# Kernel tuning notes

Measured on AMD Instinct MI355X. Metric: run time of the kernel, lower is better.

The kernel has to match this reference:

```python
import jax, jax.numpy as jnp
import numpy as np

B, L, HID = 2, 2048, 2048
H, KVH, HD = 8, 1, 256
GROUPS = H // KVH
THETA = 10000.0
NEG_INF = -1e9


def _rope_cos_sin(seq_len, hd):
    inv_freq = 1.0 / (THETA ** (jnp.arange(0, hd, 2, dtype=jnp.float32) / hd))
    t = jnp.arange(seq_len, dtype=jnp.float32)
    freqs = jnp.outer(t, inv_freq)                # [L, hd/2]
    emb = jnp.concatenate([freqs, freqs], axis=-1)  # [L, hd]
    return jnp.cos(emb), jnp.sin(emb)


def _rotate_half(x):
    x1, x2 = jnp.split(x, 2, axis=-1)
    return jnp.concatenate([-x2, x1], axis=-1)


def _apply_rope(x, cos, sin):
    # x: [B, h, L, hd]; cos/sin: [L, hd] broadcast over batch/heads
    return x * cos[None, None] + _rotate_half(x) * sin[None, None]


def setup_inputs() -> dict:
    key = jax.random.key(0)
    kx, kq, kk, kv, ko = jax.random.split(key, 5)
    s = lambda fan_in: 1.0 / np.sqrt(fan_in)
    x = jax.random.normal(kx, (B, L, HID), dtype=jnp.float32)
    Wq = jax.random.normal(kq, (HID, H * HD), dtype=jnp.float32) * s(HID)
    Wk = jax.random.normal(kk, (HID, KVH * HD), dtype=jnp.float32) * s(HID)
    Wv = jax.random.normal(kv, (HID, KVH * HD), dtype=jnp.float32) * s(HID)
    Wo = jax.random.normal(ko, (H * HD, HID), dtype=jnp.float32) * s(H * HD)
    # causal additive mask, same semantics as SDPA attn_mask (float, additive)
    causal = jnp.tril(jnp.ones((L, L), dtype=bool))
    mask = jnp.where(causal, 0.0, NEG_INF).astype(jnp.float32)[None, None]
    return {"x": x, "Wq": Wq, "Wk": Wk, "Wv": Wv, "Wo": Wo, "mask": mask}


def reference(x, Wq, Wk, Wv, Wo, mask):
    # projections -> [B, h, L, hd]
    q = (x @ Wq).reshape(B, L, H, HD).transpose(0, 2, 1, 3)
    k = (x @ Wk).reshape(B, L, KVH, HD).transpose(0, 2, 1, 3)
    v = (x @ Wv).reshape(B, L, KVH, HD).transpose(0, 2, 1, 3)
    cos, sin = _rope_cos_sin(L, HD)
    q = _apply_rope(q, cos, sin)
    k = _apply_rope(k, cos, sin)
    # GQA: replicate kv heads (repeat_interleave over head dim)
    k = jnp.repeat(k, GROUPS, axis=1)
    v = jnp.repeat(v, GROUPS, axis=1)
    scale = HD ** -0.5
    scores = jnp.einsum("bhqd,bhkd->bhqk", q, k) * scale + mask
    attn = jax.nn.softmax(scores.astype(jnp.float32), axis=-1).astype(q.dtype)
    out = jnp.einsum("bhqk,bhkd->bhqd", attn, v)
    out = out.transpose(0, 2, 1, 3).reshape(B, L, H * HD)
    return out @ Wo
```

## Files before the change

### kernel.cpp

```cpp
#include <hip/hip_runtime.h>

typedef unsigned short u16;
typedef __attribute__((ext_vector_type(8))) short short8x;
typedef __attribute__((ext_vector_type(4))) float f32x4;

#define B_ 2
#define L_ 2048
#define HID_ 2048
#define H_ 8
#define HD_ 256

__device__ __forceinline__ u16 f2bf(float f) {
  union { float f; unsigned u; } v; v.f = f;
  unsigned r = v.u + 0x7FFFu + ((v.u >> 16) & 1u);
  return (u16)(r >> 16);
}
__device__ __forceinline__ float bf2f(u16 u) {
  union { unsigned u; float f; } v; v.u = ((unsigned)u) << 16;
  return v.f;
}

__device__ __forceinline__ void gload_lds16(const void* g, void* l) {
  __builtin_amdgcn_global_load_lds((const __attribute__((address_space(1))) unsigned*)g,
                                   (__attribute__((address_space(3))) unsigned*)l, 16, 0, 0);
}

__global__ __launch_bounds__(256) void cvt_x_kernel(const float4* __restrict__ in,
                                                    u16* __restrict__ out) {
  int idx = blockIdx.x * 256 + threadIdx.x;
  float4 v = in[idx];
  u16* o = out + (size_t)idx * 4;
  o[0] = f2bf(v.x); o[1] = f2bf(v.y); o[2] = f2bf(v.z); o[3] = f2bf(v.w);
}

__global__ __launch_bounds__(256) void cvt_wt_kernel(const float* __restrict__ W,
                                                     u16* __restrict__ Wt, int K, int N) {
  __shared__ float tile[32][33];
  int n0 = blockIdx.x * 32, k0 = blockIdx.y * 32;
  int tx = threadIdx.x, ty = threadIdx.y;
#pragma unroll
  for (int i = 0; i < 32; i += 8)
    tile[ty + i][tx] = W[(size_t)(k0 + ty + i) * N + n0 + tx];
  __syncthreads();
#pragma unroll
  for (int i = 0; i < 32; i += 8)
    Wt[(size_t)(n0 + ty + i) * K + k0 + tx] = f2bf(tile[tx][ty + i]);
}

__global__ __launch_bounds__(256) void rope_kernel(const u16* __restrict__ in,
                                                   u16* __restrict__ out, int nh_shift,
                                                   int in_stride, int in_off, float scale) {
  int idx = blockIdx.x * 256 + threadIdx.x;
  int nh = 1 << nh_shift;
  int d = idx & 127;
  int t = idx >> 7;
  int h = t & (nh - 1);
  int row = t >> nh_shift;
  int l = row & (L_ - 1);
  int b = row >> 11;
  size_t ibase = (size_t)row * in_stride + in_off + h * 256 + d;
  float x1 = bf2f(in[ibase]);
  float x2 = bf2f(in[ibase + 128]);
  float f = exp2f(-(float)d * (13.287712379549449f / 128.0f));
  float ang = (float)l * f;
  float s, c;
  sincosf(ang, &s, &c);
  size_t obase = ((size_t)(b * nh + h) * L_ + l) * 256 + d;
  out[obase] = f2bf((x1 * c - x2 * s) * scale);
  out[obase + 128] = f2bf((x2 * c + x1 * s) * scale);
}

__global__ __launch_bounds__(256) void vt_kernel(const u16* __restrict__ qkvproj,
                                                 u16* __restrict__ vt) {
  __shared__ u16 tile[32][33];
  int l0 = blockIdx.x * 32, d0 = blockIdx.y * 32, b = blockIdx.z;
  int tx = threadIdx.x, ty = threadIdx.y;
#pragma unroll
  for (int i = 0; i < 32; i += 8)
    tile[ty + i][tx] = qkvproj[((size_t)b * 2048 + l0 + ty + i) * 2560 + 2304 + d0 + tx];
  __syncthreads();
#pragma unroll
  for (int i = 0; i < 32; i += 8)
    vt[((size_t)b * 256 + d0 + ty + i) * 2048 + l0 + tx] = tile[tx][ty + i];
}

template <int F32OUT>
__global__ __launch_bounds__(512) void gemm256_kernel(const u16* __restrict__ A,
                                                      const u16* __restrict__ Bt,
                                                      void* __restrict__ Cv,
                                                      int M, int N, int K) {
  __shared__ __attribute__((aligned(16))) u16 As[2][256 * 64];
  __shared__ __attribute__((aligned(16))) u16 Bs[2][256 * 64];
  const int tid = threadIdx.x, lane = tid & 63, w = tid >> 6;
  const int wr = w >> 2, wc = w & 3;
  const int l15 = lane & 15, l4 = lane >> 4;
  const int nbx = gridDim.x;
  int flat = blockIdx.y * nbx + blockIdx.x;
  int nwg = nbx * gridDim.y;
  int q8 = nwg >> 3, r8 = nwg & 7;
  int xcd = flat & 7, idx8 = flat >> 3;
  int neu = (xcd < r8 ? xcd * (q8 + 1) : r8 * (q8 + 1) + (xcd - r8) * q8) + idx8;
  const int m0 = (neu / nbx) * 256, n0 = (neu % nbx) * 256;
  const int NT = K >> 6;

  f32x4 acc[8][4] = {};
  short8x a[4][2], b[4][2];

#define STAGE_A(t, s)                                                           \
  {                                                                             \
    _Pragma("unroll") for (int i = 0; i < 4; ++i) {                             \
      int c = i * 512 + tid;                                                    \
      int row = c >> 3, j = (c & 7) ^ (row & 7);                                \
      gload_lds16(A + (size_t)(m0 + row) * K + (t) * 64 + j * 8,                \
                  (char*)&As[s][0] + (i * 512 + w * 64) * 16);                  \
    }                                                                           \
  }
#define STAGE_B(t, s)                                                           \
  {                                                                             \
    _Pragma("unroll") for (int i = 0; i < 4; ++i) {                             \
      int c = i * 512 + tid;                                                    \
      int row = c >> 3, j = (c & 7) ^ (row & 7);                                \
      gload_lds16(Bt + (size_t)(n0 + row) * K + (t) * 64 + j * 8,               \
                  (char*)&Bs[s][0] + (i * 512 + w * 64) * 16);                  \
    }                                                                           \
  }
#define RD_A(s, mi, ks)                                                         \
  (*(const short8x*)((const char*)&As[s][0] +                                   \
      ((((wr * 128 + (mi) * 16 + l15) * 128 + ((ks) * 4 + l4) * 16)) ^          \
       ((l15 & 7) << 4))))
#define RD_B(s, ni, ks)                                                         \
  (*(const short8x*)((const char*)&Bs[s][0] +                                   \
      ((((wc * 64 + (ni) * 16 + l15) * 128 + ((ks) * 4 + l4) * 16)) ^           \
       ((l15 & 7) << 4))))

  STAGE_A(0, 0);
  STAGE_B(0, 0);
  asm volatile("s_waitcnt vmcnt(0)" ::: "memory");
  __builtin_amdgcn_s_barrier();

  for (int t = 0; t < NT; ++t) {
    const int s = t & 1;
    const bool ns = (t + 1 < NT);
#pragma unroll
    for (int mi = 0; mi < 4; ++mi) { a[mi][0] = RD_A(s, mi, 0); a[mi][1] = RD_A(s, mi, 1); }
#pragma unroll
    for (int ni = 0; ni < 2; ++ni) { b[ni][0] = RD_B(s, ni, 0); b[ni][1] = RD_B(s, ni, 1); }
    if (ns) STAGE_A(t + 1, s ^ 1);
    __builtin_amdgcn_s_barrier();
    __builtin_amdgcn_s_setprio(1);
#pragma unroll
    for (int mi = 0; mi < 4; ++mi)
#pragma unroll
      for (int ni = 0; ni < 2; ++ni) {
        acc[mi][ni] = __builtin_amdgcn_mfma_f32_16x16x32_bf16(a[mi][0], b[ni][0], acc[mi][ni], 0, 0, 0);
        acc[mi][ni] = __builtin_amdgcn_mfma_f32_16x16x32_bf16(a[mi][1], b[ni][1], acc[mi][ni], 0, 0, 0);
      }
    __builtin_amdgcn_s_setprio(0);
    __builtin_amdgcn_s_barrier();
#pragma unroll
    for (int ni = 2; ni < 4; ++ni) { b[ni][0] = RD_B(s, ni, 0); b[ni][1] = RD_B(s, ni, 1); }
    if (ns) STAGE_B(t + 1, s ^ 1);
    __builtin_amdgcn_s_barrier();
    __builtin_amdgcn_s_setprio(1);
#pragma unroll
    for (int mi = 0; mi < 4; ++mi)
#pragma unroll
      for (int ni = 2; ni < 4; ++ni) {
        acc[mi][ni] = __builtin_amdgcn_mfma_f32_16x16x32_bf16(a[mi][0], b[ni][0], acc[mi][ni], 0, 0, 0);
        acc[mi][ni] = __builtin_amdgcn_mfma_f32_16x16x32_bf16(a[mi][1], b[ni][1], acc[mi][ni], 0, 0, 0);
      }
    __builtin_amdgcn_s_setprio(0);
    __builtin_amdgcn_s_barrier();
#pragma unroll
    for (int mi = 0; mi < 4; ++mi) { a[mi][0] = RD_A(s, mi + 4, 0); a[mi][1] = RD_A(s, mi + 4, 1); }
    __builtin_amdgcn_s_barrier();
    __builtin_amdgcn_s_setprio(1);
#pragma unroll
    for (int mi = 0; mi < 4; ++mi)
#pragma unroll
      for (int ni = 2; ni < 4; ++ni) {
        acc[mi + 4][ni] = __builtin_amdgcn_mfma_f32_16x16x32_bf16(a[mi][0], b[ni][0], acc[mi + 4][ni], 0, 0, 0);
        acc[mi + 4][ni] = __builtin_amdgcn_mfma_f32_16x16x32_bf16(a[mi][1], b[ni][1], acc[mi + 4][ni], 0, 0, 0);
      }
    __builtin_amdgcn_s_setprio(0);
    __builtin_amdgcn_s_barrier();
    __builtin_amdgcn_s_setprio(1);
#pragma unroll
    for (int mi = 0; mi < 4; ++mi)
#pragma unroll
      for (int ni = 0; ni < 2; ++ni) {
        acc[mi + 4][ni] = __builtin_amdgcn_mfma_f32_16x16x32_bf16(a[mi][0], b[ni][0], acc[mi + 4][ni], 0, 0, 0);
        acc[mi + 4][ni] = __builtin_amdgcn_mfma_f32_16x16x32_bf16(a[mi][1], b[ni][1], acc[mi + 4][ni], 0, 0, 0);
      }
    __builtin_amdgcn_s_setprio(0);
    if (ns) asm volatile("s_waitcnt vmcnt(0)" ::: "memory");
    __builtin_amdgcn_s_barrier();
  }
#pragma unroll
  for (int mi = 0; mi < 8; ++mi) {
#pragma unroll
    for (int ni = 0; ni < 4; ++ni) {
      int gcol = n0 + wc * 64 + ni * 16 + l15;
#pragma unroll
      for (int r = 0; r < 4; ++r) {
        int grow = m0 + wr * 128 + mi * 16 + l4 * 4 + r;
        if (F32OUT)
          ((float*)Cv)[(size_t)grow * N + gcol] = acc[mi][ni][r];
        else
          ((u16*)Cv)[(size_t)grow * N + gcol] = f2bf(acc[mi][ni][r]);
      }
    }
  }
#undef STAGE_A
#undef STAGE_B
#undef RD_A
#undef RD_B
}

__global__ __launch_bounds__(512) void flash_kernel(const u16* __restrict__ qb,
                                                    const u16* __restrict__ kb,
                                                    const u16* __restrict__ vt,
                                                    u16* __restrict__ attn_o) {
  __shared__ __attribute__((aligned(16))) u16 Kbuf[2][64 * 256];
  __shared__ __attribute__((aligned(16))) u16 Vbuf[2][256 * 64];
  __shared__ __attribute__((aligned(16))) u16 Ps[8 * 16 * 64];
  const int x = blockIdx.x;
  const int p = x >> 4;
  const int bh = x & 15;
  const int b = bh >> 3;
  const int h = bh & 7;
  const int tid = threadIdx.x, lane = tid & 63, w = tid >> 6;
  const int l15 = lane & 15, l4 = lane >> 4;
  const int j = (w < 4) ? (31 - p) : p;
  const int q0 = j * 64 + (w & 3) * 16;
  const int nt = (31 - p) + 1;

  const u16* qrow = qb + ((size_t)(b * 8 + h) * L_ + q0 + l15) * 256;
  short8x qf[8];
#pragma unroll
  for (int kc = 0; kc < 8; ++kc)
    qf[kc] = *(const short8x*)(qrow + kc * 32 + l4 * 8);

  f32x4 o[16] = {};
  float mrow = -3e38f, srow = 0.f;

  const u16* kbase = kb + (size_t)b * (L_ * 256);
  const u16* vbase = vt + (size_t)b * (256 * L_);

#define STAGE(t, s)                                                            \
  {                                                                            \
    _Pragma("unroll") for (int i2 = 0; i2 < 4; ++i2) {                         \
      int c = i2 * 512 + tid;                                                  \
      int rk = c >> 5, cck = c & 31, jk = cck ^ (rk & 7);                      \
      gload_lds16(kbase + (size_t)((t) * 64 + rk) * 256 + jk * 8,              \
                  (char*)&Kbuf[s][0] + (i2 * 512 + w * 64) * 16);              \
      int rd = c >> 3, ccv = c & 7, jv = ccv ^ (rd & 7);                       \
      gload_lds16(vbase + (size_t)rd * L_ + (t) * 64 + jv * 8,                 \
                  (char*)&Vbuf[s][0] + (i2 * 512 + w * 64) * 16);              \
    }                                                                          \
  }

  STAGE(0, 0);
  asm volatile("s_waitcnt vmcnt(0)" ::: "memory");
  __syncthreads();

  for (int t = 0; t < nt; ++t) {
    if (t + 1 < nt) STAGE(t + 1, (t + 1) & 1);
    if (t <= j) {
      const char* Kb = (const char*)&Kbuf[t & 1][0];
      const char* Vb = (const char*)&Vbuf[t & 1][0];

      f32x4 sacc[4] = {};
      __builtin_amdgcn_s_setprio(1);
#pragma unroll
      for (int kc = 0; kc < 8; ++kc)
#pragma unroll
        for (int n = 0; n < 4; ++n) {
          int row = n * 16 + l15;
          short8x kf = *(const short8x*)(Kb +
              ((row * 512 + kc * 64 + l4 * 16) ^ ((row & 7) << 4)));
          sacc[n] = __builtin_amdgcn_mfma_f32_16x16x32_bf16(kf, qf[kc], sacc[n], 0, 0, 0);
        }
      __builtin_amdgcn_s_setprio(0);
      float pp[4][4];
      const bool dm = (t == j);
      const int qg = q0 + l15;
      float pm = -3e38f;
#pragma unroll
      for (int n = 0; n < 4; ++n)
#pragma unroll
        for (int r = 0; r < 4; ++r) {
          int kvg = t * 64 + n * 16 + l4 * 4 + r;
          float v = sacc[n][r];
          if (dm && (kvg > qg)) v = -1e30f;
          pp[n][r] = v;
          pm = fmaxf(pm, v);
        }
      pm = fmaxf(pm, __shfl_xor(pm, 16));
      pm = fmaxf(pm, __shfl_xor(pm, 32));
      const bool defer = __all(pm <= mrow + 8.f);
      float mn, alpha;
      if (defer) {
        mn = mrow;
      } else {
        mn = fmaxf(mrow, pm);
        alpha = __expf(mrow - mn);
        mrow = mn;
      }
      float rs = 0.f;
#pragma unroll
      for (int n = 0; n < 4; ++n)
#pragma unroll
        for (int r = 0; r < 4; ++r) {
          pp[n][r] = __expf(pp[n][r] - mn);
          rs += pp[n][r];
        }
      rs += __shfl_xor(rs, 16);
      rs += __shfl_xor(rs, 32);
      if (defer) {
        srow += rs;
      } else {
        srow = srow * alpha + rs;
        float av[4];
#pragma unroll
        for (int r = 0; r < 4; ++r)
          av[r] = __shfl(alpha, l4 * 4 + r, 16);
#pragma unroll
        for (int ff = 0; ff < 16; ++ff) {
          o[ff][0] *= av[0]; o[ff][1] *= av[1];
          o[ff][2] *= av[2]; o[ff][3] *= av[3];
        }
      }
#pragma unroll
      for (int n = 0; n < 4; ++n)
#pragma unroll
        for (int r = 0; r < 4; r += 2) {
          unsigned pk;
          asm("v_cvt_pk_bf16_f32 %0, %1, %2" : "=v"(pk) : "v"(pp[n][r]), "v"(pp[n][r + 1]));
          *(unsigned*)((char*)Ps + w * 2048 +
                       ((l15 * 128 + (n * 16 + l4 * 4 + r) * 2) ^ ((l15 & 7) << 4))) = pk;
        }
      asm volatile("s_waitcnt lgkmcnt(0)" ::: "memory");
      short8x paf[2];
#pragma unroll
      for (int kc2 = 0; kc2 < 2; ++kc2)
        paf[kc2] = *(const short8x*)((const char*)Ps + w * 2048 +
            ((l15 * 128 + kc2 * 64 + l4 * 16) ^ ((l15 & 7) << 4)));
      __builtin_amdgcn_s_setprio(1);
#pragma unroll
      for (int kc2 = 0; kc2 < 2; ++kc2)
#pragma unroll
        for (int ff = 0; ff < 16; ++ff) {
          int rd = ff * 16 + l15;
          short8x vf = *(const short8x*)(Vb +
              ((rd * 128 + kc2 * 64 + l4 * 16) ^ ((rd & 7) << 4)));
          o[ff] = __builtin_amdgcn_mfma_f32_16x16x32_bf16(paf[kc2], vf, o[ff], 0, 0, 0);
        }
      __builtin_amdgcn_s_setprio(0);
    }
    asm volatile("s_waitcnt vmcnt(0)" ::: "memory");
    __syncthreads();
  }
  float sv[4];
#pragma unroll
  for (int r = 0; r < 4; ++r)
    sv[r] = __shfl(srow, l4 * 4 + r, 16);
#pragma unroll
  for (int r = 0; r < 4; ++r) {
    float inv = 1.0f / sv[r];
    int grow = q0 + l4 * 4 + r;
    size_t base = ((size_t)b * L_ + grow) * (size_t)(H_ * HD_) + h * 256;
#pragma unroll
    for (int ff = 0; ff < 16; ++ff)
      attn_o[base + ff * 16 + l15] = f2bf(o[ff][r] * inv);
  }
#undef STAGE
}

extern "C" void kernel_launch(void* const* d_in, const int* in_sizes, int n_in,
                              void* d_out, int out_size, void* d_ws, size_t ws_size,
                              hipStream_t stream) {
  const float* x  = (const float*)d_in[0];
  const float* Wq = (const float*)d_in[1];
  const float* Wk = (const float*)d_in[2];
  const float* Wv = (const float*)d_in[3];
  const float* Wo = (const float*)d_in[4];
  float* out = (float*)d_out;
  char* ws = (char*)d_ws;
  size_t off = 0;
  auto alloc = [&](size_t bytes) {
    void* p = ws + off;
    off = (off + bytes + 255) & ~(size_t)255;
    return p;
  };
  u16* wqkv_t  = (u16*)alloc(2560ull * 2048 * 2);
  u16* wo_t    = (u16*)alloc(2048ull * 2048 * 2);
  u16* xbf     = (u16*)alloc(4096ull * 2048 * 2);
  u16* qkvproj = (u16*)alloc(4096ull * 2560 * 2);
  u16* kb      = (u16*)alloc(4096ull * 256 * 2);
  u16* vtb     = (u16*)alloc(4096ull * 256 * 2);
  u16* qbuf    = xbf;
  u16* attn_o  = qkvproj;

  cvt_x_kernel<<<8192, 256, 0, stream>>>((const float4*)x, xbf);
  cvt_wt_kernel<<<dim3(64, 64), dim3(32, 8), 0, stream>>>(Wq, wqkv_t, 2048, 2048);
  cvt_wt_kernel<<<dim3(8, 64),  dim3(32, 8), 0, stream>>>(Wk, wqkv_t + 2048ull * 2048, 2048, 256);
  cvt_wt_kernel<<<dim3(8, 64),  dim3(32, 8), 0, stream>>>(Wv, wqkv_t + 2304ull * 2048, 2048, 256);
  cvt_wt_kernel<<<dim3(64, 64), dim3(32, 8), 0, stream>>>(Wo, wo_t, 2048, 2048);

  gemm256_kernel<0><<<dim3(10, 16), 512, 0, stream>>>(xbf, wqkv_t, qkvproj, 4096, 2560, 2048);

  rope_kernel<<<16384, 256, 0, stream>>>(qkvproj, qbuf, 3, 2560, 0, 0.0625f);
  rope_kernel<<<2048, 256, 0, stream>>>(qkvproj, kb, 0, 2560, 2048, 1.0f);
  vt_kernel<<<dim3(64, 8, 2), dim3(32, 8), 0, stream>>>(qkvproj, vtb);

  flash_kernel<<<256, 512, 0, stream>>>(qbuf, kb, vtb, attn_o);

  gemm256_kernel<1><<<dim3(8, 16), 512, 0, stream>>>(attn_o, wo_t, out, 4096, 2048, 2048);
}
```

Measured before the change: 242.0 us.

## Switch GEMMs to 256x128 tiles with triple-buffered LDS prefetch

Replaces the 256x256-tile GEMM with a 256x128 tile. The 8 waves now form a 4x2 grid, each computing a 64x64 sub-tile. Shared buffers go from double to triple buffering, so loads for tile t+2 are issued while tile t is computed, with a partial vmcnt wait. The grid doubles, giving 320 and 256 workgroups on 256 CUs instead of 160 and 128, which is meant to fill the GPU better and hide global latency. The trade-off is lower arithmetic intensity per tile, more LDS per block (144KB), and vmcnt counts that must match the number of issued loads.

```diff
diff --git a/kernel.cpp b/kernel.cpp
--- a/kernel.cpp
+++ b/kernel.cpp
@@ -85,14 +85,14 @@
 }
 
 template <int F32OUT>
-__global__ __launch_bounds__(512) void gemm256_kernel(const u16* __restrict__ A,
-                                                      const u16* __restrict__ Bt,
-                                                      void* __restrict__ Cv,
-                                                      int M, int N, int K) {
-  __shared__ __attribute__((aligned(16))) u16 As[2][256 * 64];
-  __shared__ __attribute__((aligned(16))) u16 Bs[2][256 * 64];
+__global__ __launch_bounds__(512) void gemmtb_kernel(const u16* __restrict__ A,
+                                                     const u16* __restrict__ Bt,
+                                                     void* __restrict__ Cv,
+                                                     int M, int N, int K) {
+  __shared__ __attribute__((aligned(16))) u16 As[3][256 * 64];
+  __shared__ __attribute__((aligned(16))) u16 Bs[3][128 * 64];
   const int tid = threadIdx.x, lane = tid & 63, w = tid >> 6;
-  const int wr = w >> 2, wc = w & 3;
+  const int wr = w >> 1, wc = w & 1;
   const int l15 = lane & 15, l4 = lane >> 4;
   const int nbx = gridDim.x;
   int flat = blockIdx.y * nbx + blockIdx.x;
@@ -100,10 +100,10 @@
   int q8 = nwg >> 3, r8 = nwg & 7;
   int xcd = flat & 7, idx8 = flat >> 3;
   int neu = (xcd < r8 ? xcd * (q8 + 1) : r8 * (q8 + 1) + (xcd - r8) * q8) + idx8;
-  const int m0 = (neu / nbx) * 256, n0 = (neu % nbx) * 256;
+  const int m0 = (neu / nbx) * 256, n0 = (neu % nbx) * 128;
   const int NT = K >> 6;
 
-  f32x4 acc[8][4] = {};
+  f32x4 acc[4][4] = {};
   short8x a[4][2], b[4][2];
 
 #define STAGE_A(t, s)                                                           \
@@ -117,7 +117,7 @@
   }
 #define STAGE_B(t, s)                                                           \
   {                                                                             \
-    _Pragma("unroll") for (int i = 0; i < 4; ++i) {                             \
+    _Pragma("unroll") for (int i = 0; i < 2; ++i) {                             \
       int c = i * 512 + tid;                                                    \
       int row = c >> 3, j = (c & 7) ^ (row & 7);                                \
       gload_lds16(Bt + (size_t)(n0 + row) * K + (t) * 64 + j * 8,               \
@@ -126,7 +126,7 @@
   }
 #define RD_A(s, mi, ks)                                                         \
   (*(const short8x*)((const char*)&As[s][0] +                                   \
-      ((((wr * 128 + (mi) * 16 + l15) * 128 + ((ks) * 4 + l4) * 16)) ^          \
+      ((((wr * 64 + (mi) * 16 + l15) * 128 + ((ks) * 4 + l4) * 16)) ^           \
        ((l15 & 7) << 4))))
 #define RD_B(s, ni, ks)                                                         \
   (*(const short8x*)((const char*)&Bs[s][0] +                                   \
@@ -135,17 +135,19 @@
 
   STAGE_A(0, 0);
   STAGE_B(0, 0);
-  asm volatile("s_waitcnt vmcnt(0)" ::: "memory");
+  STAGE_A(1, 1);
+  STAGE_B(1, 1);
+  asm volatile("s_waitcnt vmcnt(6)" ::: "memory");
   __builtin_amdgcn_s_barrier();
 
   for (int t = 0; t < NT; ++t) {
-    const int s = t & 1;
-    const bool ns = (t + 1 < NT);
-#pragma unroll
-    for (int mi = 0; mi < 4; ++mi) { a[mi][0] = RD_A(s, mi, 0); a[mi][1] = RD_A(s, mi, 1); }
-#pragma unroll
-    for (int ni = 0; ni < 2; ++ni) { b[ni][0] = RD_B(s, ni, 0); b[ni][1] = RD_B(s, ni, 1); }
-    if (ns) STAGE_A(t + 1, s ^ 1);
+    const int cur = t % 3, nxt = (t + 2) % 3;
+    const bool ns = (t + 2 < NT);
+#pragma unroll
+    for (int mi = 0; mi < 4; ++mi) { a[mi][0] = RD_A(cur, mi, 0); a[mi][1] = RD_A(cur, mi, 1); }
+#pragma unroll
+    for (int ni = 0; ni < 2; ++ni) { b[ni][0] = RD_B(cur, ni, 0); b[ni][1] = RD_B(cur, ni, 1); }
+    if (ns) STAGE_A(t + 2, nxt);
     __builtin_amdgcn_s_barrier();
     __builtin_amdgcn_s_setprio(1);
 #pragma unroll
@@ -158,8 +160,8 @@
     __builtin_amdgcn_s_setprio(0);
     __builtin_amdgcn_s_barrier();
 #pragma unroll
-    for (int ni = 2; ni < 4; ++ni) { b[ni][0] = RD_B(s, ni, 0); b[ni][1] = RD_B(s, ni, 1); }
-    if (ns) STAGE_B(t + 1, s ^ 1);
+    for (int ni = 2; ni < 4; ++ni) { b[ni][0] = RD_B(cur, ni, 0); b[ni][1] = RD_B(cur, ni, 1); }
+    if (ns) STAGE_B(t + 2, nxt);
     __builtin_amdgcn_s_barrier();
     __builtin_amdgcn_s_setprio(1);
 #pragma unroll
@@ -170,40 +172,18 @@
         acc[mi][ni] = __builtin_amdgcn_mfma_f32_16x16x32_bf16(a[mi][1], b[ni][1], acc[mi][ni], 0, 0, 0);
       }
     __builtin_amdgcn_s_setprio(0);
+    if (ns) asm volatile("s_waitcnt vmcnt(6)" ::: "memory");
+    else    asm volatile("s_waitcnt vmcnt(0)" ::: "memory");
     __builtin_amdgcn_s_barrier();
-#pragma unroll
-    for (int mi = 0; mi < 4; ++mi) { a[mi][0] = RD_A(s, mi + 4, 0); a[mi][1] = RD_A(s, mi + 4, 1); }
-    __builtin_amdgcn_s_barrier();
-    __builtin_amdgcn_s_setprio(1);
-#pragma unroll
-    for (int mi = 0; mi < 4; ++mi)
-#pragma unroll
-      for (int ni = 2; ni < 4; ++ni) {
-        acc[mi + 4][ni] = __builtin_amdgcn_mfma_f32_16x16x32_bf16(a[mi][0], b[ni][0], acc[mi + 4][ni], 0, 0, 0);
-        acc[mi + 4][ni] = __builtin_amdgcn_mfma_f32_16x16x32_bf16(a[mi][1], b[ni][1], acc[mi + 4][ni], 0, 0, 0);
-      }
-    __builtin_amdgcn_s_setprio(0);
-    __builtin_amdgcn_s_barrier();
-    __builtin_amdgcn_s_setprio(1);
-#pragma unroll
-    for (int mi = 0; mi < 4; ++mi)
-#pragma unroll
-      for (int ni = 0; ni < 2; ++ni) {
-        acc[mi + 4][ni] = __builtin_amdgcn_mfma_f32_16x16x32_bf16(a[mi][0], b[ni][0], acc[mi + 4][ni], 0, 0, 0);
-        acc[mi + 4][ni] = __builtin_amdgcn_mfma_f32_16x16x32_bf16(a[mi][1], b[ni][1], acc[mi + 4][ni], 0, 0, 0);
-      }
-    __builtin_amdgcn_s_setprio(0);
-    if (ns) asm volatile("s_waitcnt vmcnt(0)" ::: "memory");
-    __builtin_amdgcn_s_barrier();
-  }
-#pragma unroll
-  for (int mi = 0; mi < 8; ++mi) {
+  }
+#pragma unroll
+  for (int mi = 0; mi < 4; ++mi) {
 #pragma unroll
     for (int ni = 0; ni < 4; ++ni) {
       int gcol = n0 + wc * 64 + ni * 16 + l15;
 #pragma unroll
       for (int r = 0; r < 4; ++r) {
-        int grow = m0 + wr * 128 + mi * 16 + l4 * 4 + r;
+        int grow = m0 + wr * 64 + mi * 16 + l4 * 4 + r;
         if (F32OUT)
           ((float*)Cv)[(size_t)grow * N + gcol] = acc[mi][ni][r];
         else
@@ -408,7 +388,7 @@
   cvt_wt_kernel<<<dim3(8, 64),  dim3(32, 8), 0, stream>>>(Wv, wqkv_t + 2304ull * 2048, 2048, 256);
   cvt_wt_kernel<<<dim3(64, 64), dim3(32, 8), 0, stream>>>(Wo, wo_t, 2048, 2048);
 
-  gemm256_kernel<0><<<dim3(10, 16), 512, 0, stream>>>(xbf, wqkv_t, qkvproj, 4096, 2560, 2048);
+  gemmtb_kernel<0><<<dim3(20, 16), 512, 0, stream>>>(xbf, wqkv_t, qkvproj, 4096, 2560, 2048);
 
   rope_kernel<<<16384, 256, 0, stream>>>(qkvproj, qbuf, 3, 2560, 0, 0.0625f);
   rope_kernel<<<2048, 256, 0, stream>>>(qkvproj, kb, 0, 2560, 2048, 1.0f);
@@ -416,5 +396,5 @@
 
   flash_kernel<<<256, 512, 0, stream>>>(qbuf, kb, vtb, attn_o);
 
-  gemm256_kernel<1><<<dim3(8, 16), 512, 0, stream>>>(attn_o, wo_t, out, 4096, 2048, 2048);
-}
+  gemmtb_kernel<1><<<dim3(16, 16), 512, 0, stream>>>(attn_o, wo_t, out, 4096, 2048, 2048);
+}
```

Result: faster. 229.7 us (-5.1%).

## Split GEMM tiles into half-tiles and prefetch B two k-steps ahead

Applied to the files above, without the earlier changes.

Restructures the 256x256 GEMM kernel so the A and B LDS tiles are stored as two 128-row halves. Each half is staged at a separate point in the MFMA schedule, with B prefetched two k-steps ahead and partial vmcnt waits instead of full drains. The aim is to spread global-to-LDS traffic across the compute phases and hide load latency better, in the style of 8-phase ping-pong GEMM schedules. The cost is more complex synchronisation, where an error in the wait counts could cause reads of stale LDS data.

```diff
diff --git a/kernel.cpp b/kernel.cpp
--- a/kernel.cpp
+++ b/kernel.cpp
@@ -85,12 +85,12 @@
 }
 
 template <int F32OUT>
-__global__ __launch_bounds__(512) void gemm256_kernel(const u16* __restrict__ A,
-                                                      const u16* __restrict__ Bt,
-                                                      void* __restrict__ Cv,
-                                                      int M, int N, int K) {
-  __shared__ __attribute__((aligned(16))) u16 As[2][256 * 64];
-  __shared__ __attribute__((aligned(16))) u16 Bs[2][256 * 64];
+__global__ __launch_bounds__(512) void gemm8p_kernel(const u16* __restrict__ A,
+                                                     const u16* __restrict__ Bt,
+                                                     void* __restrict__ Cv,
+                                                     int M, int N, int K) {
+  __shared__ __attribute__((aligned(16))) u16 As[2][2][128 * 64];
+  __shared__ __attribute__((aligned(16))) u16 Bs[2][2][128 * 64];
   const int tid = threadIdx.x, lane = tid & 63, w = tid >> 6;
   const int wr = w >> 2, wc = w & 3;
   const int l15 = lane & 15, l4 = lane >> 4;
@@ -104,96 +104,102 @@
   const int NT = K >> 6;
 
   f32x4 acc[8][4] = {};
-  short8x a[4][2], b[4][2];
-
-#define STAGE_A(t, s)                                                           \
-  {                                                                             \
-    _Pragma("unroll") for (int i = 0; i < 4; ++i) {                             \
-      int c = i * 512 + tid;                                                    \
-      int row = c >> 3, j = (c & 7) ^ (row & 7);                                \
-      gload_lds16(A + (size_t)(m0 + row) * K + (t) * 64 + j * 8,                \
-                  (char*)&As[s][0] + (i * 512 + w * 64) * 16);                  \
-    }                                                                           \
-  }
-#define STAGE_B(t, s)                                                           \
-  {                                                                             \
-    _Pragma("unroll") for (int i = 0; i < 4; ++i) {                             \
-      int c = i * 512 + tid;                                                    \
-      int row = c >> 3, j = (c & 7) ^ (row & 7);                                \
-      gload_lds16(Bt + (size_t)(n0 + row) * K + (t) * 64 + j * 8,               \
-                  (char*)&Bs[s][0] + (i * 512 + w * 64) * 16);                  \
-    }                                                                           \
-  }
-#define RD_A(s, mi, ks)                                                         \
-  (*(const short8x*)((const char*)&As[s][0] +                                   \
-      ((((wr * 128 + (mi) * 16 + l15) * 128 + ((ks) * 4 + l4) * 16)) ^          \
-       ((l15 & 7) << 4))))
-#define RD_B(s, ni, ks)                                                         \
-  (*(const short8x*)((const char*)&Bs[s][0] +                                   \
-      ((((wc * 64 + (ni) * 16 + l15) * 128 + ((ks) * 4 + l4) * 16)) ^           \
-       ((l15 & 7) << 4))))
-
-  STAGE_A(0, 0);
-  STAGE_B(0, 0);
-  asm volatile("s_waitcnt vmcnt(0)" ::: "memory");
+  short8x a[4][2], blo[2][2], bhi[2][2];
+
+#define STAGE_HT(PTR, br, h, t, s, SBUF)                                          \
+  {                                                                               \
+    _Pragma("unroll") for (int i = 0; i < 2; ++i) {                               \
+      int c = i * 512 + tid;                                                      \
+      int row = c >> 3, j = (c & 7) ^ (row & 7);                                  \
+      gload_lds16(PTR + (size_t)((br) + (h) * 128 + row) * K + (t) * 64 + j * 8,  \
+                  (char*)&SBUF[s][h][0] + (i * 512 + w * 64) * 16);               \
+    }                                                                             \
+  }
+#define RD(SBUF, s, h, rowin, ks)                                                 \
+  (*(const short8x*)((const char*)&SBUF[s][h][0] +                                \
+      ((((rowin) * 128 + ((ks) * 4 + l4) * 16)) ^ (((rowin) & 7) << 4))))
+
+  const int brB = (wc & 1) * 64;
+
+  STAGE_HT(A, m0, 0, 0, 0, As);
+  STAGE_HT(A, m0, 1, 0, 0, As);
+  STAGE_HT(Bt, n0, 0, 0, 0, Bs);
+  STAGE_HT(Bt, n0, 1, 0, 0, Bs);
+  STAGE_HT(Bt, n0, 0, 1, 1, Bs);
+  STAGE_HT(Bt, n0, 1, 1, 1, Bs);
+  asm volatile("s_waitcnt vmcnt(4)" ::: "memory");
   __builtin_amdgcn_s_barrier();
 
   for (int t = 0; t < NT; ++t) {
-    const int s = t & 1;
-    const bool ns = (t + 1 < NT);
-#pragma unroll
-    for (int mi = 0; mi < 4; ++mi) { a[mi][0] = RD_A(s, mi, 0); a[mi][1] = RD_A(s, mi, 1); }
-#pragma unroll
-    for (int ni = 0; ni < 2; ++ni) { b[ni][0] = RD_B(s, ni, 0); b[ni][1] = RD_B(s, ni, 1); }
-    if (ns) STAGE_A(t + 1, s ^ 1);
+    const int s = t & 1, sn = s ^ 1;
+#pragma unroll
+    for (int mi = 0; mi < 4; ++mi) {
+      a[mi][0] = RD(As, s, wr, mi * 16 + l15, 0);
+      a[mi][1] = RD(As, s, wr, mi * 16 + l15, 1);
+    }
+#pragma unroll
+    for (int ni = 0; ni < 2; ++ni) {
+      blo[ni][0] = RD(Bs, s, wc >> 1, brB + ni * 16 + l15, 0);
+      blo[ni][1] = RD(Bs, s, wc >> 1, brB + ni * 16 + l15, 1);
+    }
+    if (t + 1 < NT) STAGE_HT(A, m0, 0, t + 1, sn, As);
     __builtin_amdgcn_s_barrier();
     __builtin_amdgcn_s_setprio(1);
 #pragma unroll
     for (int mi = 0; mi < 4; ++mi)
 #pragma unroll
       for (int ni = 0; ni < 2; ++ni) {
-        acc[mi][ni] = __builtin_amdgcn_mfma_f32_16x16x32_bf16(a[mi][0], b[ni][0], acc[mi][ni], 0, 0, 0);
-        acc[mi][ni] = __builtin_amdgcn_mfma_f32_16x16x32_bf16(a[mi][1], b[ni][1], acc[mi][ni], 0, 0, 0);
+        acc[mi][ni] = __builtin_amdgcn_mfma_f32_16x16x32_bf16(a[mi][0], blo[ni][0], acc[mi][ni], 0, 0, 0);
+        acc[mi][ni] = __builtin_amdgcn_mfma_f32_16x16x32_bf16(a[mi][1], blo[ni][1], acc[mi][ni], 0, 0, 0);
       }
     __builtin_amdgcn_s_setprio(0);
     __builtin_amdgcn_s_barrier();
 #pragma unroll
-    for (int ni = 2; ni < 4; ++ni) { b[ni][0] = RD_B(s, ni, 0); b[ni][1] = RD_B(s, ni, 1); }
-    if (ns) STAGE_B(t + 1, s ^ 1);
+    for (int ni = 0; ni < 2; ++ni) {
+      bhi[ni][0] = RD(Bs, s, wc >> 1, brB + 32 + ni * 16 + l15, 0);
+      bhi[ni][1] = RD(Bs, s, wc >> 1, brB + 32 + ni * 16 + l15, 1);
+    }
+    if (t + 1 < NT) STAGE_HT(A, m0, 1, t + 1, sn, As);
     __builtin_amdgcn_s_barrier();
     __builtin_amdgcn_s_setprio(1);
 #pragma unroll
     for (int mi = 0; mi < 4; ++mi)
 #pragma unroll
-      for (int ni = 2; ni < 4; ++ni) {
-        acc[mi][ni] = __builtin_amdgcn_mfma_f32_16x16x32_bf16(a[mi][0], b[ni][0], acc[mi][ni], 0, 0, 0);
-        acc[mi][ni] = __builtin_amdgcn_mfma_f32_16x16x32_bf16(a[mi][1], b[ni][1], acc[mi][ni], 0, 0, 0);
+      for (int ni = 0; ni < 2; ++ni) {
+        acc[mi][2 + ni] = __builtin_amdgcn_mfma_f32_16x16x32_bf16(a[mi][0], bhi[ni][0], acc[mi][2 + ni], 0, 0, 0);
+        acc[mi][2 + ni] = __builtin_amdgcn_mfma_f32_16x16x32_bf16(a[mi][1], bhi[ni][1], acc[mi][2 + ni], 0, 0, 0);
       }
     __builtin_amdgcn_s_setprio(0);
     __builtin_amdgcn_s_barrier();
 #pragma unroll
-    for (int mi = 0; mi < 4; ++mi) { a[mi][0] = RD_A(s, mi + 4, 0); a[mi][1] = RD_A(s, mi + 4, 1); }
+    for (int mi = 0; mi < 4; ++mi) {
+      a[mi][0] = RD(As, s, wr, 64 + mi * 16 + l15, 0);
+      a[mi][1] = RD(As, s, wr, 64 + mi * 16 + l15, 1);
+    }
+    if (t + 2 < NT) STAGE_HT(Bt, n0, 0, t + 2, s, Bs);
     __builtin_amdgcn_s_barrier();
     __builtin_amdgcn_s_setprio(1);
 #pragma unroll
     for (int mi = 0; mi < 4; ++mi)
 #pragma unroll
-      for (int ni = 2; ni < 4; ++ni) {
-        acc[mi + 4][ni] = __builtin_amdgcn_mfma_f32_16x16x32_bf16(a[mi][0], b[ni][0], acc[mi + 4][ni], 0, 0, 0);
-        acc[mi + 4][ni] = __builtin_amdgcn_mfma_f32_16x16x32_bf16(a[mi][1], b[ni][1], acc[mi + 4][ni], 0, 0, 0);
+      for (int ni = 0; ni < 2; ++ni) {
+        acc[4 + mi][2 + ni] = __builtin_amdgcn_mfma_f32_16x16x32_bf16(a[mi][0], bhi[ni][0], acc[4 + mi][2 + ni], 0, 0, 0);
+        acc[4 + mi][2 + ni] = __builtin_amdgcn_mfma_f32_16x16x32_bf16(a[mi][1], bhi[ni][1], acc[4 + mi][2 + ni], 0, 0, 0);
       }
     __builtin_amdgcn_s_setprio(0);
     __builtin_amdgcn_s_barrier();
+    if (t + 2 < NT) STAGE_HT(Bt, n0, 1, t + 2, s, Bs);
     __builtin_amdgcn_s_setprio(1);
 #pragma unroll
     for (int mi = 0; mi < 4; ++mi)
 #pragma unroll
       for (int ni = 0; ni < 2; ++ni) {
-        acc[mi + 4][ni] = __builtin_amdgcn_mfma_f32_16x16x32_bf16(a[mi][0], b[ni][0], acc[mi + 4][ni], 0, 0, 0);
-        acc[mi + 4][ni] = __builtin_amdgcn_mfma_f32_16x16x32_bf16(a[mi][1], b[ni][1], acc[mi + 4][ni], 0, 0, 0);
+        acc[4 + mi][ni] = __builtin_amdgcn_mfma_f32_16x16x32_bf16(a[mi][0], blo[ni][0], acc[4 + mi][ni], 0, 0, 0);
+        acc[4 + mi][ni] = __builtin_amdgcn_mfma_f32_16x16x32_bf16(a[mi][1], blo[ni][1], acc[4 + mi][ni], 0, 0, 0);
       }
     __builtin_amdgcn_s_setprio(0);
-    if (ns) asm volatile("s_waitcnt vmcnt(0)" ::: "memory");
+    if (t + 2 < NT) asm volatile("s_waitcnt vmcnt(4)" ::: "memory");
+    else            asm volatile("s_waitcnt vmcnt(0)" ::: "memory");
     __builtin_amdgcn_s_barrier();
   }
 #pragma unroll
@@ -211,10 +217,8 @@
       }
     }
   }
-#undef STAGE_A
-#undef STAGE_B
-#undef RD_A
-#undef RD_B
+#undef STAGE_HT
+#undef RD
 }
 
 __global__ __launch_bounds__(512) void flash_kernel(const u16* __restrict__ qb,
@@ -408,7 +412,7 @@
   cvt_wt_kernel<<<dim3(8, 64),  dim3(32, 8), 0, stream>>>(Wv, wqkv_t + 2304ull * 2048, 2048, 256);
   cvt_wt_kernel<<<dim3(64, 64), dim3(32, 8), 0, stream>>>(Wo, wo_t, 2048, 2048);
 
-  gemm256_kernel<0><<<dim3(10, 16), 512, 0, stream>>>(xbf, wqkv_t, qkvproj, 4096, 2560, 2048);
+  gemm8p_kernel<0><<<dim3(10, 16), 512, 0, stream>>>(xbf, wqkv_t, qkvproj, 4096, 2560, 2048);
 
   rope_kernel<<<16384, 256, 0, stream>>>(qkvproj, qbuf, 3, 2560, 0, 0.0625f);
   rope_kernel<<<2048, 256, 0, stream>>>(qkvproj, kb, 0, 2560, 2048, 1.0f);
@@ -416,5 +420,5 @@
 
   flash_kernel<<<256, 512, 0, stream>>>(qbuf, kb, vtb, attn_o);
 
-  gemm256_kernel<1><<<dim3(8, 16), 512, 0, stream>>>(attn_o, wo_t, out, 4096, 2048, 2048);
-}
+  gemm8p_kernel<1><<<dim3(8, 16), 512, 0, stream>>>(attn_o, wo_t, out, 4096, 2048, 2048);
+}
```

New measurement: 233.9 us. 1.03x faster.
